# Performance work log

Hardware: AMD Instinct MI355X
Metric: run time of the kernel (lower is better)

The kernel has to match this reference:

```python
import jax, jax.numpy as jnp
import numpy as np

D_MODEL = 2048
NUM_HEADS = 16
D_K = D_MODEL // NUM_HEADS


def setup_inputs() -> dict:
    key = jax.random.key(0)
    ks = jax.random.split(key, 9)
    s = 1.0 / np.sqrt(D_MODEL)
    return {
        "x": jax.random.normal(ks[0], (2, 2048, D_MODEL), dtype=jnp.float32),
        "Wq": jax.random.normal(ks[1], (D_MODEL, D_MODEL), dtype=jnp.float32) * s,
        "bq": jax.random.normal(ks[2], (D_MODEL,), dtype=jnp.float32) * 0.01,
        "Wk": jax.random.normal(ks[3], (D_MODEL, D_MODEL), dtype=jnp.float32) * s,
        "bk": jax.random.normal(ks[4], (D_MODEL,), dtype=jnp.float32) * 0.01,
        "Wv": jax.random.normal(ks[5], (D_MODEL, D_MODEL), dtype=jnp.float32) * s,
        "bv": jax.random.normal(ks[6], (D_MODEL,), dtype=jnp.float32) * 0.01,
        "Wo": jax.random.normal(ks[7], (D_MODEL, D_MODEL), dtype=jnp.float32) * s,
        "bo": jax.random.normal(ks[8], (D_MODEL,), dtype=jnp.float32) * 0.01,
    }


def reference(x, Wq, bq, Wk, bk, Wv, bv, Wo, bo):
    B, T, C = x.shape
    H, Dk = NUM_HEADS, D_K
    # projections (torch Linear: y = x @ W^T + b; here weights stored as [in,out])
    q = (x @ Wq + bq).reshape(B, T, H, Dk).transpose(0, 2, 1, 3)  # [B,H,T,Dk]
    k = (x @ Wk + bk).reshape(B, T, H, Dk).transpose(0, 2, 1, 3)
    v = (x @ Wv + bv).reshape(B, T, H, Dk).transpose(0, 2, 1, 3)
    score = jnp.einsum("bhqd,bhkd->bhqk", q, k) / jnp.sqrt(jnp.float32(Dk))
    attn = jax.nn.softmax(score, axis=-1)
    out = jnp.einsum("bhqk,bhkd->bhqd", attn, v)  # [B,H,T,Dk]
    out = out.transpose(0, 2, 1, 3).reshape(B, T, C)
    return out @ Wo + bo
```

## Files before the change

kernel.cpp:

```cpp
#include <hip/hip_runtime.h>
#include <cstdint>

typedef _Float16 f16;
typedef __attribute__((ext_vector_type(4))) _Float16 f16x4;
typedef __attribute__((ext_vector_type(8))) _Float16 f16x8;
typedef __attribute__((ext_vector_type(4))) float f32x4;

#define DM   2048
#define TSEQ 2048
#define NB   2
#define NH   16
#define DKH  128
#define LOG2E 1.44269504088896f

__device__ __forceinline__ void gload_lds16(const void* g, void* l) {
  __builtin_amdgcn_global_load_lds((const __attribute__((address_space(1))) void*)g,
                                   (__attribute__((address_space(3))) void*)l, 16, 0, 0);
}

#define SBAR()  { asm volatile("s_barrier" ::: "memory"); __builtin_amdgcn_sched_barrier(0); }
#define LGKM0() { asm volatile("s_waitcnt lgkmcnt(0)" ::: "memory"); __builtin_amdgcn_sched_barrier(0); }
#define VMCNT0() { asm volatile("s_waitcnt vmcnt(0)" ::: "memory"); __builtin_amdgcn_sched_barrier(0); }

__global__ __launch_bounds__(256) void cvt_kernel(const float* __restrict__ src,
                                                  f16* __restrict__ dst, int n8) {
  int i = blockIdx.x * 256 + threadIdx.x;
  if (i >= n8) return;
  const float4* s = (const float4*)src + 2 * (size_t)i;
  float4 a = s[0], b = s[1];
  f16x8 o;
  o[0]=(f16)a.x; o[1]=(f16)a.y; o[2]=(f16)a.z; o[3]=(f16)a.w;
  o[4]=(f16)b.x; o[5]=(f16)b.y; o[6]=(f16)b.z; o[7]=(f16)b.w;
  ((f16x8*)dst)[i] = o;
}

__global__ __launch_bounds__(256) void wt_kernel(const float* __restrict__ W0, const float* __restrict__ W1,
                                                 const float* __restrict__ W2, const float* __restrict__ W3,
                                                 f16* __restrict__ Dqkv, f16* __restrict__ Dout) {
  __shared__ f16 S[64 * 80];
  int z = blockIdx.z;
  const float* W = (z == 0) ? W0 : (z == 1) ? W1 : (z == 2) ? W2 : W3;
  f16* D = (z < 3) ? (Dqkv + (size_t)z * DM * DM) : Dout;
  int n0 = blockIdx.x * 64, k0 = blockIdx.y * 64;
  int tid = threadIdx.x;
#pragma unroll
  for (int i = 0; i < 4; i++) {
    int flat = i * 256 + tid;
    int r = flat >> 4, c4 = flat & 15;
    float4 v = *(const float4*)(W + (size_t)(k0 + r) * DM + n0 + c4 * 4);
    S[(c4 * 4 + 0) * 80 + r] = (f16)v.x;
    S[(c4 * 4 + 1) * 80 + r] = (f16)v.y;
    S[(c4 * 4 + 2) * 80 + r] = (f16)v.z;
    S[(c4 * 4 + 3) * 80 + r] = (f16)v.w;
  }
  __syncthreads();
#pragma unroll
  for (int i = 0; i < 2; i++) {
    int flat = i * 256 + tid;
    int nl = flat >> 3, kc = flat & 7;
    f16x8 v = *(const f16x8*)&S[nl * 80 + kc * 8];
    *(f16x8*)(D + (size_t)(n0 + nl) * DM + k0 + kc * 8) = v;
  }
}

template <int MODE>
__global__ __launch_bounds__(512, 2) void gemm_kernel(const f16* __restrict__ A, const f16* __restrict__ Bt,
                                                      const float* __restrict__ b0, const float* __restrict__ b1,
                                                      const float* __restrict__ b2,
                                                      f16* __restrict__ Oh, float* __restrict__ Of) {
  constexpr int BN   = (MODE == 0) ? 192 : 128;
  constexpr int NFR  = BN / 64;
  constexpr int WN   = BN / 4;
  constexpr int NXB  = (MODE == 0) ? 32 : 16;
  constexpr int CPX  = (16 * NXB) / 8;
  __shared__ __align__(16) f16 As[2][256 * 64];
  __shared__ __align__(16) f16 Bs[2][NFR * 64 * 64];
  const int K = DM;
  const int NT = K / 64;
  const int NITER = NT / 2;
  int tid = threadIdx.x, l = tid & 63, w = tid >> 6;
  int lo = l & 15, hi = l >> 4;
  int wm = w >> 2, wn = w & 3;
  int lin = blockIdx.x;
  int swz = (lin & 7) * CPX + (lin >> 3);
  int by = swz & 15, bx = swz >> 4;
  int m0 = by * 256, n0 = bx * BN;

  const f16* Ag = A + (size_t)m0 * K;
  const f16* Bg = Bt + (size_t)n0 * K;

  auto stageAu = [&](int b, int u, int t) {
    int rin = (w << 3) + (l >> 3);
    int csw = (l & 7) ^ (rin & 7);
    gload_lds16(Ag + (size_t)(u * 64 + rin) * K + t * 64 + csw * 8,
                &As[b][u * 4096 + w * 512]);
  };
  auto stageBu = [&](int b, int u, int t) {
    int rin = (w << 3) + (l >> 3);
    int csw = (l & 7) ^ (rin & 7);
    gload_lds16(Bg + (size_t)(u * 64 + rin) * K + t * 64 + csw * 8,
                &Bs[b][u * 4096 + w * 512]);
  };
  auto stageAll = [&](int b, int t) {
#pragma unroll
    for (int u = 0; u < 4; u++) stageAu(b, u, t);
#pragma unroll
    for (int u = 0; u < NFR; u++) stageBu(b, u, t);
  };

  f32x4 acc[8][NFR] = {};
  f16x8 bfr[NFR][2];
  f16x8 af[4][2][2];

#define READ_BFR(b)                                                                 \
  {                                                                                 \
    _Pragma("unroll")                                                               \
    for (int ni = 0; ni < NFR; ni++) {                                              \
      int row = wn * WN + ni * 16 + lo;                                             \
      bfr[ni][0] = *(const f16x8*)&Bs[b][row * 64 + (((0 + hi) ^ (row & 7)) << 3)]; \
      bfr[ni][1] = *(const f16x8*)&Bs[b][row * 64 + (((4 + hi) ^ (row & 7)) << 3)]; \
    }                                                                               \
  }

#define READ_AF(b, q)                                                               \
  {                                                                                 \
    _Pragma("unroll")                                                               \
    for (int e = 0; e < 2; e++) {                                                   \
      int row = wm * 128 + ((q) * 2 + e) * 16 + lo;                                 \
      af[q][e][0] = *(const f16x8*)&As[b][row * 64 + (((0 + hi) ^ (row & 7)) << 3)]; \
      af[q][e][1] = *(const f16x8*)&As[b][row * 64 + (((4 + hi) ^ (row & 7)) << 3)]; \
    }                                                                               \
  }

#define MFMA_Q(q)                                                                   \
    __builtin_amdgcn_s_setprio(1);                                                  \
    _Pragma("unroll")                                                               \
    for (int e = 0; e < 2; e++)                                                     \
      _Pragma("unroll")                                                             \
      for (int ni = 0; ni < NFR; ni++) {                                            \
        acc[(q)*2+e][ni] = __builtin_amdgcn_mfma_f32_16x16x32_f16(af[q][e][0], bfr[ni][0], acc[(q)*2+e][ni], 0, 0, 0); \
        acc[(q)*2+e][ni] = __builtin_amdgcn_mfma_f32_16x16x32_f16(af[q][e][1], bfr[ni][1], acc[(q)*2+e][ni], 0, 0, 0); \
      }                                                                             \
    __builtin_amdgcn_s_setprio(0);

#define VMCNT_P()                                                                   \
    if constexpr (MODE == 0) { asm volatile("s_waitcnt vmcnt(7)" ::: "memory"); }   \
    else                     { asm volatile("s_waitcnt vmcnt(6)" ::: "memory"); }   \
    __builtin_amdgcn_sched_barrier(0);

  stageAll(0, 0);
  stageAll(1, 1);
  VMCNT_P();
  SBAR();
  READ_BFR(0); READ_AF(0, 0);

#pragma unroll 1
  for (int it = 0; it < NITER; ++it) {
    int t2 = (2 * it + 2 < NT) ? 2 * it + 2 : NT - 1;
    int t3 = (2 * it + 3 < NT) ? 2 * it + 3 : NT - 1;

    MFMA_Q(0); READ_AF(0, 1);
    MFMA_Q(1); READ_AF(0, 2);
    MFMA_Q(2); READ_AF(0, 3);
    LGKM0();
    VMCNT0();
    SBAR();
    stageAll(0, t2);
    MFMA_Q(3);
    __builtin_amdgcn_sched_barrier(0);
    READ_BFR(1); READ_AF(1, 0);

    MFMA_Q(0); READ_AF(1, 1);
    MFMA_Q(1); READ_AF(1, 2);
    MFMA_Q(2); READ_AF(1, 3);
    LGKM0();
    VMCNT0();
    SBAR();
    stageAll(1, t3);
    MFMA_Q(3);
    __builtin_amdgcn_sched_barrier(0);
    READ_BFR(0); READ_AF(0, 0);
  }
  asm volatile("s_waitcnt vmcnt(0) lgkmcnt(0)" ::: "memory");

#pragma unroll
  for (int mi = 0; mi < 8; mi++) {
    int gm = m0 + wm * 128 + mi * 16 + (hi << 2);
#pragma unroll
    for (int ni = 0; ni < NFR; ni++) {
      int gn = n0 + wn * WN + ni * 16 + lo;
      if (MODE == 0) {
        int proj = gn >> 11, nn = gn & 2047;
        const float* bp = (proj == 0) ? b0 : (proj == 1) ? b1 : b2;
        float bias = bp[nn];
        int h = nn >> 7, d = nn & 127;
        int b = gm >> 11;
        int t0 = gm & 2047;
        if (proj < 2) {
#pragma unroll
          for (int r = 0; r < 4; r++) {
            Oh[(size_t)proj * ((size_t)NB * NH * TSEQ * DKH) +
               (((size_t)(b * NH + h) * TSEQ + t0 + r) * DKH) + d] = (f16)(acc[mi][ni][r] + bias);
          }
        } else {
          f16x4 pk;
#pragma unroll
          for (int r = 0; r < 4; r++) pk[r] = (f16)(acc[mi][ni][r] + bias);
          *(f16x4*)(Oh + 2ull * ((size_t)NB * NH * TSEQ * DKH) +
                    ((size_t)(b * NH + h) * DKH + d) * TSEQ + t0) = pk;
        }
      } else {
        float bias = b0[gn];
#pragma unroll
        for (int r = 0; r < 4; r++)
          Of[(size_t)(gm + r) * DM + gn] = acc[mi][ni][r] + bias;
      }
    }
  }
#undef READ_BFR
#undef READ_AF
#undef MFMA_Q
#undef VMCNT_P
}

__global__ __launch_bounds__(256, 2) void attn_kernel(const f16* __restrict__ Qb, const f16* __restrict__ Kb,
                                                      const f16* __restrict__ Vtb, f16* __restrict__ AO) {
  __shared__ f16 Ks[2][64 * 128];
  __shared__ f16 Vt[128 * 64];
  __shared__ f16 Ps[4][32 * 72];
  int tid = threadIdx.x, l = tid & 63, w = tid >> 6;
  int lo = l & 15, hi = l >> 4;
  int lin = blockIdx.x;
  int xcd = lin & 7, slot = lin >> 3;
  int bh = xcd * 4 + (slot & 3), qt = slot >> 2;
  const float CSC = 0.12753257f;
  const float THR = 62.0f;
  const f16* Qg = Qb + (size_t)bh * TSEQ * DKH;
  const f16* Kg = Kb + (size_t)bh * TSEQ * DKH;
  const f16* Vg = Vtb + (size_t)bh * DKH * TSEQ;

  auto stageK = [&](int kt, int b) {
#pragma unroll
    for (int i = 0; i < 4; i++) {
      int chunk = (w * 4 + i) * 64 + l;
      int rowk = chunk >> 4, c = chunk & 15;
      int csw = c ^ (rowk & 15);
      gload_lds16(Kg + (size_t)(kt * 64 + rowk) * DKH + csw * 8, &Ks[b][(w * 4 + i) * 512]);
    }
  };
  auto stageV = [&](int kt) {
#pragma unroll
    for (int i = 0; i < 4; i++) {
      int chunk = (w * 4 + i) * 64 + l;
      int d = chunk >> 3, c = chunk & 7;
      int csw = c ^ (d & 7);
      gload_lds16(Vg + (size_t)d * TSEQ + kt * 64 + csw * 8, &Vt[(w * 4 + i) * 512]);
    }
  };

  f16x8 aq[2][4];
#pragma unroll
  for (int hf = 0; hf < 2; hf++) {
    int qrow = qt * 128 + w * 32 + hf * 16 + lo;
#pragma unroll
    for (int c = 0; c < 4; c++)
      aq[hf][c] = *(const f16x8*)(Qg + (size_t)qrow * DKH + c * 32 + (hi << 3));
  }

  f32x4 o[2][8] = {};
  float mrow[2] = {-INFINITY, -INFINITY};
  float lrow[2] = {0.f, 0.f};

  stageK(0, 0);
  VMCNT0();
  SBAR();

#pragma unroll 1
  for (int ktile = 0; ktile < TSEQ / 64; ++ktile) {
    int c = ktile & 1;
    int tn = (ktile + 1 < TSEQ / 64) ? ktile + 1 : TSEQ / 64 - 1;

    stageK(tn, c ^ 1);
    stageV(ktile);

    f32x4 s[2][4] = {};
    __builtin_amdgcn_s_setprio(1);
#pragma unroll
    for (int ks = 0; ks < 4; ++ks) {
      int ktl = ks * 16 + lo;
#pragma unroll
      for (int cq = 0; cq < 4; cq++) {
        int cc = (cq * 4 + hi) ^ lo;
        f16x8 bk = *(const f16x8*)&Ks[c][ktl * 128 + cc * 8];
        s[0][ks] = __builtin_amdgcn_mfma_f32_16x16x32_f16(bk, aq[0][cq], s[0][ks], 0, 0, 0);
        s[1][ks] = __builtin_amdgcn_mfma_f32_16x16x32_f16(bk, aq[1][cq], s[1][ks], 0, 0, 0);
      }
    }
    __builtin_amdgcn_s_setprio(0);

#pragma unroll
    for (int hf = 0; hf < 2; hf++) {
      float mk[4];
#pragma unroll
      for (int ks = 0; ks < 4; ks++)
        mk[ks] = fmaxf(fmaxf(s[hf][ks][0], s[hf][ks][1]), fmaxf(s[hf][ks][2], s[hf][ks][3]));
      float mt = fmaxf(fmaxf(mk[0], mk[1]), fmaxf(mk[2], mk[3]));
      mt = fmaxf(mt, __shfl_xor(mt, 16));
      mt = fmaxf(mt, __shfl_xor(mt, 32));

      if (__any(mt > mrow[hf] + THR)) {
        float mn = fmaxf(mrow[hf], mt);
        float al = exp2f((mrow[hf] - mn) * CSC);
        mrow[hf] = mn;
        lrow[hf] *= al;
        float alr[4];
#pragma unroll
        for (int r = 0; r < 4; r++) alr[r] = __shfl(al, (hi << 2) + r);
#pragma unroll
        for (int dsub = 0; dsub < 8; dsub++)
#pragma unroll
          for (int r = 0; r < 4; r++) o[hf][dsub][r] *= alr[r];
      }

      float mCn = -mrow[hf] * CSC;
      float sum = 0.f;
#pragma unroll
      for (int ks = 0; ks < 4; ks++) {
        f16x4 pk;
        float part = 0.f;
#pragma unroll
        for (int r = 0; r < 4; r++) {
          float p = exp2f(__builtin_fmaf(s[hf][ks][r], CSC, mCn));
          pk[r] = (f16)p;
          part += p;
        }
        sum += part;
        *(f16x4*)&Ps[w][(hf * 16 + lo) * 72 + ks * 16 + (hi << 2)] = pk;
      }
      sum += __shfl_xor(sum, 16);
      sum += __shfl_xor(sum, 32);
      lrow[hf] += sum;
    }

    LGKM0();
    VMCNT0();

    f16x8 pa[2][2];
#pragma unroll
    for (int hf = 0; hf < 2; hf++)
#pragma unroll
      for (int kk = 0; kk < 2; kk++)
        pa[hf][kk] = *(const f16x8*)&Ps[w][(hf * 16 + lo) * 72 + kk * 32 + (hi << 3)];
    __builtin_amdgcn_s_setprio(1);
#pragma unroll
    for (int kk = 0; kk < 2; kk++) {
#pragma unroll
      for (int dsub = 0; dsub < 8; dsub++) {
        int d = dsub * 16 + lo;
        f16x8 vf = *(const f16x8*)&Vt[d * 64 + (((kk * 4 + hi) ^ (d & 7)) << 3)];
        o[0][dsub] = __builtin_amdgcn_mfma_f32_16x16x32_f16(pa[0][kk], vf, o[0][dsub], 0, 0, 0);
        o[1][dsub] = __builtin_amdgcn_mfma_f32_16x16x32_f16(pa[1][kk], vf, o[1][dsub], 0, 0, 0);
      }
    }
    __builtin_amdgcn_s_setprio(0);

    LGKM0();
    SBAR();
  }

  int b = bh >> 4, h = bh & 15;
#pragma unroll
  for (int hf = 0; hf < 2; hf++) {
    float inv = 1.0f / lrow[hf];
    float invr[4];
#pragma unroll
    for (int r = 0; r < 4; r++) invr[r] = __shfl(inv, (hi << 2) + r);
#pragma unroll
    for (int r = 0; r < 4; r++) {
      int t = qt * 128 + w * 32 + hf * 16 + (hi << 2) + r;
      f16* dst = AO + ((size_t)b * TSEQ + t) * DM + h * DKH;
#pragma unroll
      for (int dsub = 0; dsub < 8; dsub++)
        dst[dsub * 16 + lo] = (f16)(o[hf][dsub][r] * invr[r]);
    }
  }
}

extern "C" void kernel_launch(void* const* d_in, const int* in_sizes, int n_in,
                              void* d_out, int out_size, void* d_ws, size_t ws_size,
                              hipStream_t stream) {
  const float* x  = (const float*)d_in[0];
  const float* Wq = (const float*)d_in[1];
  const float* bq = (const float*)d_in[2];
  const float* Wk = (const float*)d_in[3];
  const float* bk = (const float*)d_in[4];
  const float* Wv = (const float*)d_in[5];
  const float* bv = (const float*)d_in[6];
  const float* Wo = (const float*)d_in[7];
  const float* bo = (const float*)d_in[8];

  f16* ws    = (f16*)d_ws;
  f16* xb    = ws;
  f16* WtQKV = ws + 8388608ull;
  f16* WtO   = ws + 20971520ull;
  f16* Q     = ws + 25165824ull;
  f16* Kp    = ws + 33554432ull;
  f16* Vp    = ws + 41943040ull;
  f16* AO    = xb;

  cvt_kernel<<<4096, 256, 0, stream>>>(x, xb, (NB * TSEQ * DM) / 8);
  wt_kernel<<<dim3(32, 32, 4), 256, 0, stream>>>(Wq, Wk, Wv, Wo, WtQKV, WtO);
  gemm_kernel<0><<<512, 512, 0, stream>>>(xb, WtQKV, bq, bk, bv, Q, nullptr);
  attn_kernel<<<512, 256, 0, stream>>>(Q, Kp, Vp, AO);
  gemm_kernel<1><<<256, 512, 0, stream>>>(AO, WtO, bo, nullptr, nullptr, nullptr, (float*)d_out);
}
```

Baseline: 265.0 us.

## Software-pipeline attention loop: compute next QK^T while softmaxing current tile

Restructures the flash-attention inner loop so the QK^T MFMAs for tile t+1 are issued before the softmax of tile t, using two score register sets (s0/s1) and a manual unroll by two. K is prefetched two tiles ahead, and the full vmcnt(0) waits are replaced with partial vmcnt(4)/vmcnt(8) waits. The goal is to overlap MFMA work with the exp/reduction VALU work and to hide global-load latency. In exchange it uses more registers, which may lower occupancy, and the hand-counted vmcnt values must match the number of loads issued by stageK/stageV.

```diff
diff --git a/kernel.cpp b/kernel.cpp
--- a/kernel.cpp
+++ b/kernel.cpp
@@ -21,6 +21,8 @@
 #define SBAR()  { asm volatile("s_barrier" ::: "memory"); __builtin_amdgcn_sched_barrier(0); }
 #define LGKM0() { asm volatile("s_waitcnt lgkmcnt(0)" ::: "memory"); __builtin_amdgcn_sched_barrier(0); }
 #define VMCNT0() { asm volatile("s_waitcnt vmcnt(0)" ::: "memory"); __builtin_amdgcn_sched_barrier(0); }
+#define VMCNT4() { asm volatile("s_waitcnt vmcnt(4)" ::: "memory"); __builtin_amdgcn_sched_barrier(0); }
+#define VMCNT8() { asm volatile("s_waitcnt vmcnt(8)" ::: "memory"); __builtin_amdgcn_sched_barrier(0); }
 
 __global__ __launch_bounds__(256) void cvt_kernel(const float* __restrict__ src,
                                                   f16* __restrict__ dst, int n8) {
@@ -270,102 +272,126 @@
   f32x4 o[2][8] = {};
   float mrow[2] = {-INFINITY, -INFINITY};
   float lrow[2] = {0.f, 0.f};
+  f32x4 s0[2][4], s1[2][4];
+
+#define QK_BLOCK(SN, KB)                                                            \
+  {                                                                                 \
+    _Pragma("unroll")                                                               \
+    for (int ks = 0; ks < 4; ++ks) {                                                \
+      f32x4 z = {0.f, 0.f, 0.f, 0.f};                                               \
+      SN[0][ks] = z; SN[1][ks] = z;                                                 \
+    }                                                                               \
+    __builtin_amdgcn_s_setprio(1);                                                  \
+    _Pragma("unroll")                                                               \
+    for (int ks = 0; ks < 4; ++ks) {                                                \
+      int ktl = ks * 16 + lo;                                                       \
+      _Pragma("unroll")                                                             \
+      for (int cq = 0; cq < 4; cq++) {                                              \
+        int cc = (cq * 4 + hi) ^ lo;                                                \
+        f16x8 bk = *(const f16x8*)&Ks[KB][ktl * 128 + cc * 8];                      \
+        SN[0][ks] = __builtin_amdgcn_mfma_f32_16x16x32_f16(bk, aq[0][cq], SN[0][ks], 0, 0, 0); \
+        SN[1][ks] = __builtin_amdgcn_mfma_f32_16x16x32_f16(bk, aq[1][cq], SN[1][ks], 0, 0, 0); \
+      }                                                                             \
+    }                                                                               \
+    __builtin_amdgcn_s_setprio(0);                                                  \
+  }
+
+#define SM_BLOCK(SC)                                                                \
+  {                                                                                 \
+    _Pragma("unroll")                                                               \
+    for (int hf = 0; hf < 2; hf++) {                                                \
+      float mk[4];                                                                  \
+      _Pragma("unroll")                                                             \
+      for (int ks = 0; ks < 4; ks++)                                                \
+        mk[ks] = fmaxf(fmaxf(SC[hf][ks][0], SC[hf][ks][1]), fmaxf(SC[hf][ks][2], SC[hf][ks][3])); \
+      float mt = fmaxf(fmaxf(mk[0], mk[1]), fmaxf(mk[2], mk[3]));                   \
+      mt = fmaxf(mt, __shfl_xor(mt, 16));                                           \
+      mt = fmaxf(mt, __shfl_xor(mt, 32));                                           \
+      if (__any(mt > mrow[hf] + THR)) {                                             \
+        float mn = fmaxf(mrow[hf], mt);                                             \
+        float al = exp2f((mrow[hf] - mn) * CSC);                                    \
+        mrow[hf] = mn;                                                              \
+        lrow[hf] *= al;                                                             \
+        float alr[4];                                                               \
+        _Pragma("unroll")                                                           \
+        for (int r = 0; r < 4; r++) alr[r] = __shfl(al, (hi << 2) + r);             \
+        _Pragma("unroll")                                                           \
+        for (int dsub = 0; dsub < 8; dsub++)                                        \
+          _Pragma("unroll")                                                         \
+          for (int r = 0; r < 4; r++) o[hf][dsub][r] *= alr[r];                     \
+      }                                                                             \
+      float mCn = -mrow[hf] * CSC;                                                  \
+      float sum = 0.f;                                                              \
+      _Pragma("unroll")                                                             \
+      for (int ks = 0; ks < 4; ks++) {                                              \
+        f16x4 pk;                                                                   \
+        float part = 0.f;                                                           \
+        _Pragma("unroll")                                                           \
+        for (int r = 0; r < 4; r++) {                                               \
+          float p = exp2f(__builtin_fmaf(SC[hf][ks][r], CSC, mCn));                 \
+          pk[r] = (f16)p;                                                           \
+          part += p;                                                                \
+        }                                                                           \
+        sum += part;                                                                \
+        *(f16x4*)&Ps[w][(hf * 16 + lo) * 72 + ks * 16 + (hi << 2)] = pk;            \
+      }                                                                             \
+      sum += __shfl_xor(sum, 16);                                                   \
+      sum += __shfl_xor(sum, 32);                                                   \
+      lrow[hf] += sum;                                                              \
+    }                                                                               \
+  }
+
+#define PV_BLOCK()                                                                  \
+  {                                                                                 \
+    f16x8 pa[2][2];                                                                 \
+    _Pragma("unroll")                                                               \
+    for (int hf = 0; hf < 2; hf++)                                                  \
+      _Pragma("unroll")                                                             \
+      for (int kk = 0; kk < 2; kk++)                                                \
+        pa[hf][kk] = *(const f16x8*)&Ps[w][(hf * 16 + lo) * 72 + kk * 32 + (hi << 3)]; \
+    __builtin_amdgcn_s_setprio(1);                                                  \
+    _Pragma("unroll")                                                               \
+    for (int kk = 0; kk < 2; kk++) {                                                \
+      _Pragma("unroll")                                                             \
+      for (int dsub = 0; dsub < 8; dsub++) {                                        \
+        int d = dsub * 16 + lo;                                                     \
+        f16x8 vf = *(const f16x8*)&Vt[d * 64 + (((kk * 4 + hi) ^ (d & 7)) << 3)];   \
+        o[0][dsub] = __builtin_amdgcn_mfma_f32_16x16x32_f16(pa[0][kk], vf, o[0][dsub], 0, 0, 0); \
+        o[1][dsub] = __builtin_amdgcn_mfma_f32_16x16x32_f16(pa[1][kk], vf, o[1][dsub], 0, 0, 0); \
+      }                                                                             \
+    }                                                                               \
+    __builtin_amdgcn_s_setprio(0);                                                  \
+  }
+
+#define ATTN_ITER(t, SC, SN, KB_NEXT, KB_STAGE)                                     \
+  {                                                                                 \
+    int t2c = ((t) + 2 < 32) ? (t) + 2 : 31;                                        \
+    stageV(t);                                                                      \
+    stageK(t2c, KB_STAGE);                                                          \
+    VMCNT8();                           \
+    QK_BLOCK(SN, KB_NEXT);                                                          \
+    __builtin_amdgcn_sched_barrier(0);                                              \
+    SM_BLOCK(SC);                                                                   \
+    LGKM0();                                         \
+    VMCNT4();                              \
+    PV_BLOCK();                                                                     \
+    LGKM0();                                            \
+    SBAR();             \
+  }
 
   stageK(0, 0);
-  VMCNT0();
+  stageK(1, 1);
+  VMCNT4();
   SBAR();
+  QK_BLOCK(s0, 0);
+  LGKM0();
+  SBAR();
 
 #pragma unroll 1
-  for (int ktile = 0; ktile < TSEQ / 64; ++ktile) {
-    int c = ktile & 1;
-    int tn = (ktile + 1 < TSEQ / 64) ? ktile + 1 : TSEQ / 64 - 1;
-
-    stageK(tn, c ^ 1);
-    stageV(ktile);
-
-    f32x4 s[2][4] = {};
-    __builtin_amdgcn_s_setprio(1);
-#pragma unroll
-    for (int ks = 0; ks < 4; ++ks) {
-      int ktl = ks * 16 + lo;
-#pragma unroll
-      for (int cq = 0; cq < 4; cq++) {
-        int cc = (cq * 4 + hi) ^ lo;
-        f16x8 bk = *(const f16x8*)&Ks[c][ktl * 128 + cc * 8];
-        s[0][ks] = __builtin_amdgcn_mfma_f32_16x16x32_f16(bk, aq[0][cq], s[0][ks], 0, 0, 0);
-        s[1][ks] = __builtin_amdgcn_mfma_f32_16x16x32_f16(bk, aq[1][cq], s[1][ks], 0, 0, 0);
-      }
-    }
-    __builtin_amdgcn_s_setprio(0);
-
-#pragma unroll
-    for (int hf = 0; hf < 2; hf++) {
-      float mk[4];
-#pragma unroll
-      for (int ks = 0; ks < 4; ks++)
-        mk[ks] = fmaxf(fmaxf(s[hf][ks][0], s[hf][ks][1]), fmaxf(s[hf][ks][2], s[hf][ks][3]));
-      float mt = fmaxf(fmaxf(mk[0], mk[1]), fmaxf(mk[2], mk[3]));
-      mt = fmaxf(mt, __shfl_xor(mt, 16));
-      mt = fmaxf(mt, __shfl_xor(mt, 32));
-
-      if (__any(mt > mrow[hf] + THR)) {
-        float mn = fmaxf(mrow[hf], mt);
-        float al = exp2f((mrow[hf] - mn) * CSC);
-        mrow[hf] = mn;
-        lrow[hf] *= al;
-        float alr[4];
-#pragma unroll
-        for (int r = 0; r < 4; r++) alr[r] = __shfl(al, (hi << 2) + r);
-#pragma unroll
-        for (int dsub = 0; dsub < 8; dsub++)
-#pragma unroll
-          for (int r = 0; r < 4; r++) o[hf][dsub][r] *= alr[r];
-      }
-
-      float mCn = -mrow[hf] * CSC;
-      float sum = 0.f;
-#pragma unroll
-      for (int ks = 0; ks < 4; ks++) {
-        f16x4 pk;
-        float part = 0.f;
-#pragma unroll
-        for (int r = 0; r < 4; r++) {
-          float p = exp2f(__builtin_fmaf(s[hf][ks][r], CSC, mCn));
-          pk[r] = (f16)p;
-          part += p;
-        }
-        sum += part;
-        *(f16x4*)&Ps[w][(hf * 16 + lo) * 72 + ks * 16 + (hi << 2)] = pk;
-      }
-      sum += __shfl_xor(sum, 16);
-      sum += __shfl_xor(sum, 32);
-      lrow[hf] += sum;
-    }
-
-    LGKM0();
-    VMCNT0();
-
-    f16x8 pa[2][2];
-#pragma unroll
-    for (int hf = 0; hf < 2; hf++)
-#pragma unroll
-      for (int kk = 0; kk < 2; kk++)
-        pa[hf][kk] = *(const f16x8*)&Ps[w][(hf * 16 + lo) * 72 + kk * 32 + (hi << 3)];
-    __builtin_amdgcn_s_setprio(1);
-#pragma unroll
-    for (int kk = 0; kk < 2; kk++) {
-#pragma unroll
-      for (int dsub = 0; dsub < 8; dsub++) {
-        int d = dsub * 16 + lo;
-        f16x8 vf = *(const f16x8*)&Vt[d * 64 + (((kk * 4 + hi) ^ (d & 7)) << 3)];
-        o[0][dsub] = __builtin_amdgcn_mfma_f32_16x16x32_f16(pa[0][kk], vf, o[0][dsub], 0, 0, 0);
-        o[1][dsub] = __builtin_amdgcn_mfma_f32_16x16x32_f16(pa[1][kk], vf, o[1][dsub], 0, 0, 0);
-      }
-    }
-    __builtin_amdgcn_s_setprio(0);
-
-    LGKM0();
-    SBAR();
+  for (int tp = 0; tp < 16; ++tp) {
+    int t = 2 * tp;
+    ATTN_ITER(t,     s0, s1, 1, 0);
+    ATTN_ITER(t + 1, s1, s0, 0, 1);
   }
 
   int b = bh >> 4, h = bh & 15;
@@ -384,6 +410,10 @@
         dst[dsub * 16 + lo] = (f16)(o[hf][dsub][r] * invr[r]);
     }
   }
+#undef QK_BLOCK
+#undef SM_BLOCK
+#undef PV_BLOCK
+#undef ATTN_ITER
 }
 
 extern "C" void kernel_launch(void* const* d_in, const int* in_sizes, int n_in,
```

Measured after the change: 263.2 us. About the same (-0.7%).
